# Kernel tuning notes

Measured on AMD Instinct MI355X. Metric: run time of the kernel, lower is better.

The kernel has to match this reference:

```python
import jax, jax.numpy as jnp
import numpy as np
import math

D = 384        # d_model
DC = 1024      # d_cut3r
NH = 8         # n_heads
NP = 4         # n_points
B, H, W = 8, 64, 64
EPS = 1e-5


def _offset_bias():
    thetas = np.arange(NH) * (2.0 * math.pi / NH)
    g = np.stack([np.cos(thetas), np.sin(thetas)], -1)
    g = g / np.abs(g).max(-1, keepdims=True)
    g = np.tile(g[:, None, :], (1, NP, 1)) * ((np.arange(NP) + 1.0) / NP)[None, :, None]
    return jnp.asarray(g.reshape(-1), jnp.float32)


def _ln(x, g, b):
    m = x.mean(-1, keepdims=True)
    v = ((x - m) ** 2).mean(-1, keepdims=True)
    return (x - m) * jax.lax.rsqrt(v + EPS) * g + b


def _grid_sample(img, grid):
    # img: [N, C, Hk, Wk]; grid: [N, Q, P, 2] with (x, y) in [-1, 1]
    # torch F.grid_sample semantics: bilinear, padding_mode='zeros', align_corners=False
    N, C, Hk, Wk = img.shape
    ix = ((grid[..., 0] + 1.0) * Wk - 1.0) * 0.5   # [N,Q,P] pixel coords
    iy = ((grid[..., 1] + 1.0) * Hk - 1.0) * 0.5
    x0 = jnp.floor(ix); y0 = jnp.floor(iy)
    wx1 = ix - x0; wx0 = 1.0 - wx1
    wy1 = iy - y0; wy0 = 1.0 - wy1
    flat = img.reshape(N, C, Hk * Wk)

    def corner(xf, yf, wgt):
        valid = (xf >= 0) & (xf < Wk) & (yf >= 0) & (yf < Hk)
        xi = jnp.clip(xf, 0, Wk - 1).astype(jnp.int32)
        yi = jnp.clip(yf, 0, Hk - 1).astype(jnp.int32)
        idx = (yi * Wk + xi).reshape(N, 1, -1)  # [N,1,Q*P]
        v = jnp.take_along_axis(flat, jnp.broadcast_to(idx, (N, C, idx.shape[-1])), axis=2)
        v = v.reshape(N, C, xf.shape[1], xf.shape[2])               # [N,C,Q,P]
        w = (wgt * valid.astype(img.dtype))[:, None]                # [N,1,Q,P]
        return v * w

    return (corner(x0, y0, wx0 * wy0) + corner(x0 + 1.0, y0, wx1 * wy0)
            + corner(x0, y0 + 1.0, wx0 * wy1) + corner(x0 + 1.0, y0 + 1.0, wx1 * wy1))


def setup_inputs() -> dict:
    key = jax.random.key(0)
    ks = jax.random.split(key, 16)
    rn = lambda k, shape: jax.random.normal(k, shape, jnp.float32) * 0.02
    return {
        'visual_feat': jax.random.normal(ks[0], (B, D, H, W), jnp.float32),
        'cut3r_features': jax.random.normal(ks[1], (B, 730, DC), jnp.float32),
        'ln_v_g': jnp.ones((D,), jnp.float32), 'ln_v_b': jnp.zeros((D,), jnp.float32),
        'ln_c_g': jnp.ones((DC,), jnp.float32), 'ln_c_b': jnp.zeros((DC,), jnp.float32),
        'W_c1': rn(ks[2], (DC, 2 * D)), 'b_c1': jnp.zeros((2 * D,), jnp.float32),
        'W_c2': rn(ks[3], (2 * D, D)), 'b_c2': jnp.zeros((D,), jnp.float32),
        'W_off': rn(ks[4], (D, NH * NP * 2)), 'b_off': _offset_bias(),
        'W_attn': rn(ks[5], (D, NH * NP)), 'b_attn': jnp.zeros((NH * NP,), jnp.float32),
        'W_out': rn(ks[6], (D, D)), 'b_out': jnp.zeros((D,), jnp.float32),
        'W_f1': rn(ks[7], (D, 4 * D)), 'b_f1': jnp.zeros((4 * D,), jnp.float32),
        'W_f2': rn(ks[8], (4 * D, D)), 'b_f2': jnp.zeros((D,), jnp.float32),
        'W_g1': rn(ks[9], (D, D // 4)), 'b_g1': jnp.zeros((D // 4,), jnp.float32),
        'W_g2': rn(ks[10], (D // 4, 1)), 'b_g2': jnp.full((1,), -5.0, jnp.float32),
        'ln_o_g': jnp.ones((D,), jnp.float32), 'ln_o_b': jnp.zeros((D,), jnp.float32),
    }


def reference(visual_feat, cut3r_features, ln_v_g, ln_v_b, ln_c_g, ln_c_b,
              W_c1, b_c1, W_c2, b_c2, W_off, b_off, W_attn, b_attn,
              W_out, b_out, W_f1, b_f1, W_f2, b_f2, W_g1, b_g1, W_g2, b_g2,
              ln_o_g, ln_o_b):
    Bb, C, Hh, Ww = visual_feat.shape
    Nq = Hh * Ww
    dh = C // NH
    vflat = visual_feat.reshape(Bb, C, Nq).transpose(0, 2, 1)            # [B,Nq,C]
    vn = _ln(vflat, ln_v_g, ln_v_b)
    cn = _ln(cut3r_features, ln_c_g, ln_c_b)
    cp = jax.nn.gelu(cn @ W_c1 + b_c1, approximate=False) @ W_c2 + b_c2  # [B,730,C]
    grid = cp[:, 1:, :].reshape(Bb, 27, 27, C).transpose(0, 3, 1, 2)     # [B,C,27,27]
    off = (vn @ W_off + b_off).reshape(Bb, Nq, NH, NP, 2)
    aw = jax.nn.softmax((vn @ W_attn + b_attn).reshape(Bb, Nq, NH, NP), axis=-1)
    loc = 2.0 * jax.nn.sigmoid(off) - 1.0                                # [-1,1]
    loc = loc.transpose(0, 2, 1, 3, 4).reshape(Bb * NH, Nq, NP, 2)
    value = grid.reshape(Bb * NH, dh, 27, 27)
    samp = _grid_sample(value, loc).reshape(Bb, NH, dh, Nq, NP)
    out = (samp * aw.transpose(0, 2, 1, 3)[:, :, None]).sum(-1)          # [B,NH,dh,Nq]
    out = out.transpose(0, 3, 1, 2).reshape(Bb, Nq, C)
    attn_out = out @ W_out + b_out
    ffn = jax.nn.gelu(attn_out @ W_f1 + b_f1, approximate=False) @ W_f2 + b_f2
    gate = jax.nn.sigmoid(jax.nn.relu(vflat @ W_g1 + b_g1) @ W_g2 + b_g2)  # [B,Nq,1]
    fused = _ln(vflat + gate * ffn, ln_o_g, ln_o_b)
    fused = fused.transpose(0, 2, 1).reshape(Bb, C, Hh, Ww)
    return fused, gate
```

## Files before the change

### kernel.cpp

```cpp
#include <hip/hip_runtime.h>
#include <hip/hip_bf16.h>
#include <math.h>

#define B_   8
#define D_   384
#define DC_  1024
#define NH_  8
#define NP_  4
#define DH_  48
#define NQ_  4096
#define NT_  730
#define NG_  729
#define GW_  27

typedef unsigned short u16;
typedef __attribute__((ext_vector_type(8))) short s8bf;
typedef __attribute__((ext_vector_type(4))) float f32x4;

__device__ __forceinline__ float bf2f(u16 u) { return __uint_as_float(((unsigned)u) << 16); }
__device__ __forceinline__ u16 f2bf(float f) {
    __hip_bfloat16 h = __float2bfloat16(f);
    return *reinterpret_cast<u16*>(&h);
}
__device__ __forceinline__ float rd(const float* p) { return *p; }
__device__ __forceinline__ float rd(const u16* p)   { return bf2f(*p); }
__device__ __forceinline__ void  wr(float* p, float v) { *p = v; }
__device__ __forceinline__ void  wr(u16* p, float v)   { *p = f2bf(v); }
__device__ __forceinline__ void fmacc4(float4& o, const float4 v, float w) {
    o.x = fmaf(v.x, w, o.x); o.y = fmaf(v.y, w, o.y);
    o.z = fmaf(v.z, w, o.z); o.w = fmaf(v.w, w, o.w);
}
__device__ __forceinline__ int imin(int a, int b) { return a < b ? a : b; }
__device__ __forceinline__ float fast_gelu(float x) {
    float z = 1.5957691216057308f * fmaf(0.044715f * x, x * x, x);
    return x / (1.f + __expf(-z));
}
__device__ __forceinline__ float fast_sigmoid(float x) {
    return 1.f / (1.f + __expf(-x));
}

#define GLOAD16(gp, lp) \
    __builtin_amdgcn_global_load_lds( \
        (const __attribute__((address_space(1))) void*)(gp), \
        (__attribute__((address_space(3))) void*)(lp), 16, 0, 0)

template <typename Tin, typename Tout>
__global__ __launch_bounds__(256) void transpose_kernel(
    const Tin* __restrict__ src, Tout* __restrict__ dst, int R, int Cc)
{
    __shared__ float tile[32][33];
    const int b  = blockIdx.z;
    const int c0 = blockIdx.x << 5;
    const int r0 = blockIdx.y << 5;
    const Tin*  s = src + (size_t)b * R * Cc;
    Tout*       d = dst + (size_t)b * R * Cc;
    const int tx = threadIdx.x & 31, ty = threadIdx.x >> 5;
#pragma unroll
    for (int i = 0; i < 32; i += 8)
        tile[ty + i][tx] = rd(s + (size_t)(r0 + ty + i) * Cc + c0 + tx);
    __syncthreads();
#pragma unroll
    for (int i = 0; i < 32; i += 8)
        wr(d + (size_t)(c0 + ty + i) * R + r0 + tx, tile[tx][ty + i]);
}

__global__ __launch_bounds__(256) void tr_ln_kernel(
    const float* __restrict__ visual,
    const float* __restrict__ g, const float* __restrict__ be,
    u16* __restrict__ vflat, u16* __restrict__ vn)
{
    __shared__ float lds[D_][33];
    __shared__ float sM[32], sR[32];
    const int blk = blockIdx.x;
    const int b = blk >> 7, q0 = (blk & 127) << 5;
    const int t = threadIdx.x;
    const int tx = t & 31, ty = t >> 5;
    const float* vb = visual + (size_t)b * D_ * NQ_ + q0;
#pragma unroll
    for (int ct = 0; ct < 12; ++ct)
#pragma unroll
        for (int i = 0; i < 32; i += 8) {
            const int c = ct * 32 + ty + i;
            lds[c][tx] = vb[(size_t)c * NQ_ + tx];
        }
    __syncthreads();
    const int wv = t >> 6, lane = t & 63;
    for (int k = 0; k < 8; ++k) {
        const int q = wv * 8 + k;
        float s = 0.f, ss = 0.f;
#pragma unroll
        for (int e = 0; e < 6; ++e) {
            float v = lds[lane * 6 + e][q];
            s += v; ss += v * v;
        }
#pragma unroll
        for (int o = 32; o > 0; o >>= 1) { s += __shfl_down(s, o); ss += __shfl_down(ss, o); }
        if (lane == 0) {
            float m = s / (float)D_;
            sM[q] = m; sR[q] = rsqrtf(ss / (float)D_ - m * m + 1e-5f);
        }
    }
    __syncthreads();
    for (int idx = t; idx < 32 * D_; idx += 256) {
        const int q = idx / D_, c = idx % D_;
        const float raw = lds[c][q];
        const size_t row = (size_t)b * NQ_ + q0 + q;
        vflat[row * D_ + c] = f2bf(raw);
        vn[row * D_ + c]    = f2bf((raw - sM[q]) * sR[q] * g[c] + be[c]);
    }
}

struct WtD { const float* src; u16* dst; int R; int C; int start; };
struct WtArgs { WtD d[8]; };

__global__ __launch_bounds__(256) void wt_convert_kernel(WtArgs a)
{
    __shared__ float tile[32][33];
    const int bt = blockIdx.x;
    int wi = 0;
#pragma unroll
    for (int k = 1; k < 8; ++k) if (bt >= a.d[k].start) wi = k;
    const float* src = a.d[wi].src;
    u16*         dst = a.d[wi].dst;
    const int R = a.d[wi].R, C = a.d[wi].C;
    const int local = bt - a.d[wi].start;
    const int tilesX = C >> 5;
    const int c0 = (local % tilesX) << 5;
    const int r0 = (local / tilesX) << 5;
    const int tx = threadIdx.x & 31, ty = threadIdx.x >> 5;
#pragma unroll
    for (int i = 0; i < 32; i += 8)
        tile[ty + i][tx] = src[(size_t)(r0 + ty + i) * C + c0 + tx];
    __syncthreads();
#pragma unroll
    for (int i = 0; i < 32; i += 8)
        dst[(size_t)(c0 + ty + i) * R + r0 + tx] = f2bf(tile[tx][ty + i]);
}

__global__ __launch_bounds__(256) void ln_kernel(
    const float* __restrict__ x, const float* __restrict__ g, const float* __restrict__ be,
    u16* __restrict__ out, int width)
{
    __shared__ float buf[1024];
    __shared__ float red[4][2];
    const size_t row = blockIdx.x;
    const float* xr = x + row * width;
    const int t = threadIdx.x;
    float s = 0.f, ss = 0.f;
    for (int i = t; i < width; i += 256) {
        float v = xr[i]; buf[i] = v; s += v; ss += v * v;
    }
#pragma unroll
    for (int o = 32; o > 0; o >>= 1) { s += __shfl_down(s, o); ss += __shfl_down(ss, o); }
    const int wave = t >> 6, lane = t & 63;
    if (lane == 0) { red[wave][0] = s; red[wave][1] = ss; }
    __syncthreads();
    if (t == 0) {
        float S = 0.f, SS = 0.f;
        for (int w = 0; w < 4; ++w) { S += red[w][0]; SS += red[w][1]; }
        float m = S / width;
        float v = SS / width - m * m;
        red[0][0] = m; red[0][1] = rsqrtf(v + 1e-5f);
    }
    __syncthreads();
    const float m = red[0][0], rs = red[0][1];
    u16* op = out + row * width;
    for (int i = t; i < width; i += 256)
        op[i] = f2bf((buf[i] - m) * rs * g[i] + be[i]);
}

template <int ACT, typename Tout>
__global__ __launch_bounds__(256) void mfma_gemm(
    const u16* __restrict__ A, const u16* __restrict__ Wt,
    const float* __restrict__ bias, Tout* __restrict__ C,
    int M, int N, int K)
{
    __shared__ __align__(16) u16 smem[16384];
    const int t    = threadIdx.x;
    const int m0   = blockIdx.x * 128;
    const int n0   = blockIdx.y * 128;
    const int lane = t & 63;
    const int wv   = t >> 6;
    const int wm   = (wv >> 1) * 64;
    const int wn   = (wv & 1) * 64;
    const int lr   = lane & 15;
    const int lks  = lane >> 4;

    const int nbase = wv * 64 + lane;
    const u16* aS[2]; const u16* bS[2];
#pragma unroll
    for (int j = 0; j < 2; ++j) {
        const int n   = j * 256 + nbase;
        const int row = n >> 2;
        const int src = (n & 3) ^ ((row >> 1) & 3);
        aS[j] = A  + (size_t)imin(m0 + row, M - 1) * K + src * 8;
        bS[j] = Wt + (size_t)imin(n0 + row, N - 1) * K + src * 8;
    }
    const int doff = (wv * 64) * 8;

    f32x4 acc[4][4] = {};
    const int nt = K >> 5;

#pragma unroll
    for (int j = 0; j < 2; ++j) {
        GLOAD16(aS[j], &smem[j * 2048 + doff]);
        GLOAD16(bS[j], &smem[4096 + j * 2048 + doff]);
    }
    if (nt > 1) {
#pragma unroll
        for (int j = 0; j < 2; ++j) {
            GLOAD16(aS[j] + 32, &smem[8192 + j * 2048 + doff]);
            GLOAD16(bS[j] + 32, &smem[8192 + 4096 + j * 2048 + doff]);
        }
    }

    for (int ti = 0; ti < nt; ++ti) {
        if (ti + 1 < nt) {
            asm volatile("s_waitcnt vmcnt(4)" ::: "memory");
        } else {
            asm volatile("s_waitcnt vmcnt(0)" ::: "memory");
        }
        __builtin_amdgcn_s_barrier();

        const int cb = (ti & 1) * 8192;
        const u16* Ab = &smem[cb];
        const u16* Bb = &smem[cb + 4096];
        s8bf af[4], bfr[4];
#pragma unroll
        for (int i = 0; i < 4; ++i) {
            const int ra = wm + i * 16 + lr;
            const int rb = wn + i * 16 + lr;
            af[i]  = *reinterpret_cast<const s8bf*>(
                &Ab[(size_t)((ra << 2) | (lks ^ ((ra >> 1) & 3))) * 8]);
            bfr[i] = *reinterpret_cast<const s8bf*>(
                &Bb[(size_t)((rb << 2) | (lks ^ ((rb >> 1) & 3))) * 8]);
        }
#pragma unroll
        for (int i = 0; i < 4; ++i)
#pragma unroll
            for (int j = 0; j < 4; ++j)
                acc[i][j] = __builtin_amdgcn_mfma_f32_16x16x32_bf16(af[i], bfr[j], acc[i][j], 0, 0, 0);

        __builtin_amdgcn_s_barrier();

        if (ti + 2 < nt) {
            const int k2 = (ti + 2) << 5;
#pragma unroll
            for (int j = 0; j < 2; ++j) {
                GLOAD16(aS[j] + k2, &smem[cb + j * 2048 + doff]);
                GLOAD16(bS[j] + k2, &smem[cb + 4096 + j * 2048 + doff]);
            }
        }
    }

    if constexpr (sizeof(Tout) == 2) {
        u16* Cs = smem;
#pragma unroll
        for (int i = 0; i < 4; ++i)
#pragma unroll
            for (int j = 0; j < 4; ++j) {
                const int col = wn + j * 16 + lr;
                const float bb = bias[n0 + col];
#pragma unroll
                for (int r = 0; r < 4; ++r) {
                    const int row = wm + i * 16 + (lane >> 4) * 4 + r;
                    float v = acc[i][j][r] + bb;
                    if (ACT == 1) v = fast_gelu(v);
                    if (ACT == 2) v = v > 0.f ? v : 0.f;
                    const int xr = ((((row >> 2) & 3) ^ (row & 3)) << 4);
                    Cs[(row << 7) | (col ^ xr)] = f2bf(v);
                }
            }
        __syncthreads();
        u16* Cp = reinterpret_cast<u16*>(C);
#pragma unroll
        for (int it = 0; it < 8; ++it) {
            const int row = (t >> 4) + it * 16;
            const int gr  = m0 + row;
            const int q   = (t & 15) * 8;
            const int xr  = ((((row >> 2) & 3) ^ (row & 3)) << 4);
            s8bf v = *reinterpret_cast<const s8bf*>(&Cs[(row << 7) | (q ^ xr)]);
            if (gr < M)
                *reinterpret_cast<s8bf*>(Cp + (size_t)gr * N + n0 + q) = v;
        }
    } else {
#pragma unroll
        for (int i = 0; i < 4; ++i) {
            const int gr0 = m0 + wm + i * 16 + (lane >> 4) * 4;
#pragma unroll
            for (int j = 0; j < 4; ++j) {
                const int gc = n0 + wn + j * 16 + lr;
                if (gc >= N) continue;
                const float bb = bias[gc];
#pragma unroll
                for (int r = 0; r < 4; ++r) {
                    const int gr = gr0 + r;
                    if (gr >= M) continue;
                    float v = acc[i][j][r] + bb;
                    if (ACT == 1) v = fast_gelu(v);
                    if (ACT == 2) v = v > 0.f ? v : 0.f;
                    wr(C + (size_t)gr * N + gc, v);
                }
            }
        }
    }
}

__global__ __launch_bounds__(128) void concat_bias_kernel(
    const float* __restrict__ b_off, const float* __restrict__ b_attn,
    float* __restrict__ b_cat)
{
    const int t = threadIdx.x;
    if (t < 64) b_cat[t] = b_off[t];
    else if (t < 96) b_cat[t] = b_attn[t - 64];
}

__global__ __launch_bounds__(256) void sample_kernel(
    const float* __restrict__ proj, const float* __restrict__ cpf,
    u16* __restrict__ out)
{
    __shared__ float4 sW[8][32];
    __shared__ int4   sT[8][32];

    const int blk = blockIdx.x;
    const int b   = blk / (NQ_ / 8);
    const int q0  = (blk % (NQ_ / 8)) * 8;
    const int t   = threadIdx.x;

    {
        const int qq = t >> 5, i = t & 31;
        const int h = i >> 2, p = i & 3;
        const size_t row = (size_t)b * NQ_ + q0 + qq;
        const float* pr = proj + row * 96;
        const float* lg = pr + 64 + h * 4;
        float l0 = lg[0], l1 = lg[1], l2 = lg[2], l3 = lg[3];
        float mx = fmaxf(fmaxf(l0, l1), fmaxf(l2, l3));
        float e0 = __expf(l0 - mx), e1 = __expf(l1 - mx);
        float e2 = __expf(l2 - mx), e3 = __expf(l3 - mx);
        float lp = (p == 0) ? l0 : (p == 1) ? l1 : (p == 2) ? l2 : l3;
        float aw = __expf(lp - mx) / (e0 + e1 + e2 + e3);
        float ox = pr[2 * i], oy = pr[2 * i + 1];
        float gx = 2.f * fast_sigmoid(ox) - 1.f;
        float gy = 2.f * fast_sigmoid(oy) - 1.f;
        float ix = ((gx + 1.f) * (float)GW_ - 1.f) * 0.5f;
        float iy = ((gy + 1.f) * (float)GW_ - 1.f) * 0.5f;
        float x0f = floorf(ix), y0f = floorf(iy);
        float wx1 = ix - x0f, wy1 = iy - y0f;
        float wx0 = 1.f - wx1, wy0 = 1.f - wy1;
        int xi = (int)x0f, yi = (int)y0f;
        bool vx0 = (xi >= 0) & (xi < GW_), vx1 = (xi + 1 >= 0) & (xi + 1 < GW_);
        bool vy0 = (yi >= 0) & (yi < GW_), vy1 = (yi + 1 >= 0) & (yi + 1 < GW_);
        float4 w;
        w.x = (vx0 & vy0) ? aw * wx0 * wy0 : 0.f;
        w.y = (vx1 & vy0) ? aw * wx1 * wy0 : 0.f;
        w.z = (vx0 & vy1) ? aw * wx0 * wy1 : 0.f;
        w.w = (vx1 & vy1) ? aw * wx1 * wy1 : 0.f;
        int cx0 = xi < 0 ? 0 : (xi > GW_ - 1 ? GW_ - 1 : xi);
        int cx1 = xi + 1 < 0 ? 0 : (xi + 1 > GW_ - 1 ? GW_ - 1 : xi + 1);
        int cy0 = yi < 0 ? 0 : (yi > GW_ - 1 ? GW_ - 1 : yi);
        int cy1 = yi + 1 < 0 ? 0 : (yi + 1 > GW_ - 1 ? GW_ - 1 : yi + 1);
        int4 tk;
        tk.x = cy0 * GW_ + cx0; tk.y = cy0 * GW_ + cx1;
        tk.z = cy1 * GW_ + cx0; tk.w = cy1 * GW_ + cx1;
        sW[qq][i] = w; sT[qq][i] = tk;
    }
    __syncthreads();

    const float4* vb4 = reinterpret_cast<const float4*>(cpf + (size_t)b * NT_ * D_ + D_);
    for (int idx = t; idx < 8 * 96; idx += 256) {
        const int qq = idx / 96, c4 = idx % 96, h = c4 / 12;
        float4 o = make_float4(0.f, 0.f, 0.f, 0.f);
#pragma unroll
        for (int p = 0; p < NP_; ++p) {
            const int i = h * 4 + p;
            const int4   tk = sT[qq][i];
            const float4 w  = sW[qq][i];
            fmacc4(o, vb4[(size_t)tk.x * 96 + c4], w.x);
            fmacc4(o, vb4[(size_t)tk.y * 96 + c4], w.y);
            fmacc4(o, vb4[(size_t)tk.z * 96 + c4], w.z);
            fmacc4(o, vb4[(size_t)tk.w * 96 + c4], w.w);
        }
        ushort4 pk;
        pk.x = f2bf(o.x); pk.y = f2bf(o.y); pk.z = f2bf(o.z); pk.w = f2bf(o.w);
        *reinterpret_cast<ushort4*>(&out[((size_t)b * NQ_ + q0 + qq) * D_ + c4 * 4]) = pk;
    }
}

__global__ __launch_bounds__(256) void gate_reduce_kernel(
    const float* __restrict__ gh, const float* __restrict__ Wg2,
    const float* __restrict__ bg2, float* __restrict__ gate_out)
{
    const int wave = threadIdx.x >> 6, lane = threadIdx.x & 63;
    const size_t row = (size_t)blockIdx.x * 4 + wave;
    const float* h = gh + row * 96;
    float s = h[lane] * Wg2[lane];
    if (lane < 32) s += h[64 + lane] * Wg2[64 + lane];
#pragma unroll
    for (int o = 32; o > 0; o >>= 1) s += __shfl_down(s, o);
    if (lane == 0) gate_out[row] = 1.f / (1.f + expf(-(s + bg2[0])));
}

__global__ __launch_bounds__(128) void fused_ln_kernel(
    const u16* __restrict__ vflat, const float* __restrict__ gate,
    const u16* __restrict__ ffn,
    const float* __restrict__ g, const float* __restrict__ be,
    u16* __restrict__ outT)
{
    __shared__ float buf[D_];
    __shared__ float red[2][2];
    const size_t row = blockIdx.x;
    const int t = threadIdx.x;
    const float gv = gate[row];
    float s = 0.f, ss = 0.f;
    for (int i = t; i < D_; i += 128) {
        float v = bf2f(vflat[row * D_ + i]) + gv * bf2f(ffn[row * D_ + i]);
        buf[i] = v; s += v; ss += v * v;
    }
#pragma unroll
    for (int o = 32; o > 0; o >>= 1) { s += __shfl_down(s, o); ss += __shfl_down(ss, o); }
    const int wave = t >> 6, lane = t & 63;
    if (lane == 0) { red[wave][0] = s; red[wave][1] = ss; }
    __syncthreads();
    if (t == 0) {
        float S = red[0][0] + red[1][0], SS = red[0][1] + red[1][1];
        float m = S / (float)D_;
        float v = SS / (float)D_ - m * m;
        red[0][0] = m; red[0][1] = rsqrtf(v + 1e-5f);
    }
    __syncthreads();
    const float m = red[0][0], rs = red[0][1];
    u16* op = outT + row * D_;
    for (int i = t; i < D_; i += 128)
        op[i] = f2bf((buf[i] - m) * rs * g[i] + be[i]);
}

extern "C" void kernel_launch(void* const* d_in, const int* in_sizes, int n_in,
                              void* d_out, int out_size, void* d_ws, size_t ws_size,
                              hipStream_t stream)
{
    const float* visual = (const float*)d_in[0];
    const float* cut3r  = (const float*)d_in[1];
    const float* ln_v_g = (const float*)d_in[2];
    const float* ln_v_b = (const float*)d_in[3];
    const float* ln_c_g = (const float*)d_in[4];
    const float* ln_c_b = (const float*)d_in[5];
    const float* W_c1 = (const float*)d_in[6];
    const float* b_c1 = (const float*)d_in[7];
    const float* W_c2 = (const float*)d_in[8];
    const float* b_c2 = (const float*)d_in[9];
    const float* W_off = (const float*)d_in[10];
    const float* b_off = (const float*)d_in[11];
    const float* W_attn = (const float*)d_in[12];
    const float* b_attn = (const float*)d_in[13];
    const float* W_out = (const float*)d_in[14];
    const float* b_out = (const float*)d_in[15];
    const float* W_f1 = (const float*)d_in[16];
    const float* b_f1 = (const float*)d_in[17];
    const float* W_f2 = (const float*)d_in[18];
    const float* b_f2 = (const float*)d_in[19];
    const float* W_g1 = (const float*)d_in[20];
    const float* b_g1 = (const float*)d_in[21];
    const float* W_g2 = (const float*)d_in[22];
    const float* b_g2 = (const float*)d_in[23];
    const float* ln_o_g = (const float*)d_in[24];
    const float* ln_o_b = (const float*)d_in[25];

    char* ws = (char*)d_ws;
    u16*   vflat   = (u16*)(ws + 0);
    u16*   vn      = (u16*)(ws + 25165824);
    u16*   attn_out= (u16*)(ws + 25165824);
    u16*   fusedT  = (u16*)(ws + 25165824);
    u16*   chid    = (u16*)(ws + 50331648);
    u16*   dout    = (u16*)(ws + 50331648);
    u16*   ffn     = (u16*)(ws + 50331648);
    float* cpf     = (float*)(ws + 75497472);
    u16*   wt_f1b  = (u16*)(ws + 84467712);
    u16*   wt_f2b  = wt_f1b + 589824;

    float* dout_f   = (float*)d_out;
    u16*   cn       = (u16*)d_out;
    float* proj_buf = dout_f;
    float* b_cat    = dout_f + 3145728;
    float* gate_hid = dout_f;
    u16*   hidden   = (u16*)d_out;
    char*  wtp      = (char*)d_out + 25165824;
    u16* wt_c1   = (u16*)wtp;
    u16* wt_c2   = wt_c1 + 786432;
    u16* wt_out  = wt_c2 + 294912;
    u16* wt_g1   = wt_out + 147456;
    u16* wt_off  = wt_g1 + 36864;
    u16* wt_attn = wt_off + 24576;
    float* out_fused = dout_f;
    float* out_gate  = dout_f + (size_t)B_ * D_ * NQ_;

    WtArgs wa;
    int cum = 0;
    auto fill = [&](int i, const float* src, u16* dst, int R, int C) {
        wa.d[i].src = src; wa.d[i].dst = dst; wa.d[i].R = R; wa.d[i].C = C;
        wa.d[i].start = cum; cum += (R >> 5) * (C >> 5);
    };
    fill(0, W_c1,  wt_c1,  1024, 768);
    fill(1, W_c2,  wt_c2,  768,  384);
    fill(2, W_out, wt_out, 384,  384);
    fill(3, W_g1,  wt_g1,  384,  96);
    fill(4, W_off, wt_off, 384,  64);
    fill(5, W_attn,wt_attn,384,  32);
    fill(6, W_f1,  wt_f1b, 384,  1536);
    fill(7, W_f2,  wt_f2b, 1536, 384);
    hipLaunchKernelGGL(wt_convert_kernel, dim3(cum), dim3(256), 0, stream, wa);
    hipLaunchKernelGGL(concat_bias_kernel, dim3(1), dim3(128), 0, stream, b_off, b_attn, b_cat);

    hipLaunchKernelGGL(tr_ln_kernel, dim3(1024), dim3(256), 0, stream,
                       visual, ln_v_g, ln_v_b, vflat, vn);
    hipLaunchKernelGGL(ln_kernel, dim3(5840), dim3(256), 0, stream,
                       cut3r, ln_c_g, ln_c_b, cn, 1024);
    hipLaunchKernelGGL((mfma_gemm<1, u16>), dim3(46, 6), dim3(256), 0, stream,
                       cn, wt_c1, b_c1, chid, 5840, 768, 1024);
    hipLaunchKernelGGL((mfma_gemm<0, float>), dim3(46, 3), dim3(256), 0, stream,
                       chid, wt_c2, b_c2, cpf, 5840, 384, 768);
    hipLaunchKernelGGL((mfma_gemm<0, float>), dim3(256, 1), dim3(256), 0, stream,
                       vn, wt_off, b_cat, proj_buf, 32768, 96, 384);
    hipLaunchKernelGGL(sample_kernel, dim3(4096), dim3(256), 0, stream,
                       proj_buf, cpf, dout);
    hipLaunchKernelGGL((mfma_gemm<0, u16>), dim3(256, 3), dim3(256), 0, stream,
                       dout, wt_out, b_out, attn_out, 32768, 384, 384);
    hipLaunchKernelGGL((mfma_gemm<2, float>), dim3(256, 1), dim3(256), 0, stream,
                       vflat, wt_g1, b_g1, gate_hid, 32768, 96, 384);
    hipLaunchKernelGGL(gate_reduce_kernel, dim3(8192), dim3(256), 0, stream,
                       gate_hid, W_g2, b_g2, out_gate);
    for (int c = 0; c < 2; ++c) {
        hipLaunchKernelGGL((mfma_gemm<1, u16>), dim3(128, 12), dim3(256), 0, stream,
                           attn_out + (size_t)c * 16384 * 384, wt_f1b, b_f1, hidden,
                           16384, 1536, 384);
        hipLaunchKernelGGL((mfma_gemm<0, u16>), dim3(128, 3), dim3(256), 0, stream,
                           hidden, wt_f2b, b_f2, ffn + (size_t)c * 16384 * 384,
                           16384, 384, 1536);
    }
    hipLaunchKernelGGL(fused_ln_kernel, dim3(32768), dim3(128), 0, stream,
                       vflat, out_gate, ffn, ln_o_g, ln_o_b, fusedT);
    hipLaunchKernelGGL((transpose_kernel<u16, float>), dim3(12, 128, 8), dim3(256), 0, stream,
                       fusedT, out_fused, 4096, 384);
}
```

Baseline: 365.2 us.

## Add wide 128x256-tile GEMM with LDS-staged bf16 epilogue for FFN up-projection

Adds a new 512-thread MFMA GEMM kernel with a 128x256 output tile, double-buffered swizzled LDS loads, and an epilogue that stages GELU outputs through shared memory so global stores are coalesced 16-byte writes. It replaces the 128x128 GEMM for the FFN first layer (N=1536). The larger tile raises A-operand reuse and halves the grid's column blocks. The cost is a bigger LDS footprint and 64 accumulator registers per lane, which may lower occupancy.

```diff
diff --git a/kernel.cpp b/kernel.cpp
--- a/kernel.cpp
+++ b/kernel.cpp
@@ -303,6 +303,118 @@
                 }
             }
         }
+    }
+}
+
+template <int ACT>
+__global__ __launch_bounds__(512) void mfma_gemm_wide(
+    const u16* __restrict__ A, const u16* __restrict__ Wt,
+    const float* __restrict__ bias, u16* __restrict__ C,
+    int M, int N, int K)
+{
+    __shared__ __align__(16) u16 smem[32768];
+    const int t    = threadIdx.x;
+    const int m0   = blockIdx.x * 128;
+    const int n0   = blockIdx.y * 256;
+    const int lane = t & 63;
+    const int wv   = t >> 6;
+    const int wm   = (wv >> 2) * 64;
+    const int wn   = (wv & 3) * 64;
+    const int lr   = lane & 15;
+    const int lks  = lane >> 4;
+
+    const int nA = wv * 64 + lane;
+    const int rA = nA >> 2, kA = (nA & 3) ^ ((rA >> 1) & 3);
+    const u16* aS = A + (size_t)(m0 + rA) * K + kA * 8;
+    const u16* bS[2];
+#pragma unroll
+    for (int j = 0; j < 2; ++j) {
+        const int n   = j * 512 + wv * 64 + lane;
+        const int row = n >> 2;
+        const int src = (n & 3) ^ ((row >> 1) & 3);
+        bS[j] = Wt + (size_t)(n0 + row) * K + src * 8;
+    }
+    const int dA = (wv * 64) * 8;
+
+    f32x4 acc[4][4] = {};
+    const int nt = K >> 5;
+
+    GLOAD16(aS, &smem[dA]);
+#pragma unroll
+    for (int j = 0; j < 2; ++j)
+        GLOAD16(bS[j], &smem[4096 + (j * 512 + wv * 64) * 8]);
+    if (nt > 1) {
+        GLOAD16(aS + 32, &smem[12288 + dA]);
+#pragma unroll
+        for (int j = 0; j < 2; ++j)
+            GLOAD16(bS[j] + 32, &smem[12288 + 4096 + (j * 512 + wv * 64) * 8]);
+    }
+
+    for (int ti = 0; ti < nt; ++ti) {
+        if (ti + 1 < nt) {
+            asm volatile("s_waitcnt vmcnt(3)" ::: "memory");
+        } else {
+            asm volatile("s_waitcnt vmcnt(0)" ::: "memory");
+        }
+        __builtin_amdgcn_s_barrier();
+
+        const int cb = (ti & 1) * 12288;
+        const u16* Ab = &smem[cb];
+        const u16* Bb = &smem[cb + 4096];
+        s8bf af[4], bfr[4];
+#pragma unroll
+        for (int i = 0; i < 4; ++i) {
+            const int ra = wm + i * 16 + lr;
+            const int rb = wn + i * 16 + lr;
+            af[i]  = *reinterpret_cast<const s8bf*>(
+                &Ab[(size_t)((ra << 2) | (lks ^ ((ra >> 1) & 3))) * 8]);
+            bfr[i] = *reinterpret_cast<const s8bf*>(
+                &Bb[(size_t)((rb << 2) | (lks ^ ((rb >> 1) & 3))) * 8]);
+        }
+#pragma unroll
+        for (int i = 0; i < 4; ++i)
+#pragma unroll
+            for (int j = 0; j < 4; ++j)
+                acc[i][j] = __builtin_amdgcn_mfma_f32_16x16x32_bf16(af[i], bfr[j], acc[i][j], 0, 0, 0);
+
+        __builtin_amdgcn_s_barrier();
+
+        if (ti + 2 < nt) {
+            const int k2 = (ti + 2) << 5;
+            GLOAD16(aS + k2, &smem[cb + dA]);
+#pragma unroll
+            for (int j = 0; j < 2; ++j)
+                GLOAD16(bS[j] + k2, &smem[cb + 4096 + (j * 512 + wv * 64) * 8]);
+        }
+    }
+
+    u16* Cs = smem;
+#pragma unroll
+    for (int i = 0; i < 4; ++i)
+#pragma unroll
+        for (int j = 0; j < 4; ++j) {
+            const int col = wn + j * 16 + lr;
+            const float bb = bias[n0 + col];
+#pragma unroll
+            for (int r = 0; r < 4; ++r) {
+                const int row = wm + i * 16 + (lane >> 4) * 4 + r;
+                float v = acc[i][j][r] + bb;
+                if (ACT == 1) v = fast_gelu(v);
+                if (ACT == 2) v = v > 0.f ? v : 0.f;
+                const int xr = ((((row >> 2) & 3) ^ (row & 3)) << 4);
+                Cs[(row << 8) | (col ^ xr)] = f2bf(v);
+            }
+        }
+    __syncthreads();
+#pragma unroll
+    for (int it = 0; it < 8; ++it) {
+        const int row = (t >> 5) + it * 16;
+        const int gr  = m0 + row;
+        const int q   = (t & 31) * 8;
+        const int xr  = ((((row >> 2) & 3) ^ (row & 3)) << 4);
+        s8bf v = *reinterpret_cast<const s8bf*>(&Cs[(row << 8) | (q ^ xr)]);
+        if (gr < M)
+            *reinterpret_cast<s8bf*>(C + (size_t)gr * N + n0 + q) = v;
     }
 }
 
@@ -529,7 +641,7 @@
     hipLaunchKernelGGL(gate_reduce_kernel, dim3(8192), dim3(256), 0, stream,
                        gate_hid, W_g2, b_g2, out_gate);
     for (int c = 0; c < 2; ++c) {
-        hipLaunchKernelGGL((mfma_gemm<1, u16>), dim3(128, 12), dim3(256), 0, stream,
+        hipLaunchKernelGGL((mfma_gemm_wide<1>), dim3(128, 6), dim3(512), 0, stream,
                            attn_out + (size_t)c * 16384 * 384, wt_f1b, b_f1, hidden,
                            16384, 1536, 384);
         hipLaunchKernelGGL((mfma_gemm<0, u16>), dim3(128, 3), dim3(256), 0, stream,
```

Result: faster. 358.1 us (-2.0%).
